# Kernel tuning notes

Hardware: AMD Instinct MI355X
Metric: run time of the kernel (lower is better)

Reference implementation:

```python
import jax, jax.numpy as jnp
import numpy as np

DIM = 512
N = 131072


def _linear_params(key, dim):
    # torch nn.Linear default init: U(-1/sqrt(in), 1/sqrt(in)) for W and b
    kw, kb = jax.random.split(key)
    bound = 1.0 / np.sqrt(dim)
    W = jax.random.uniform(kw, (dim, dim), jnp.float32, -bound, bound)
    b = jax.random.uniform(kb, (dim,), jnp.float32, -bound, bound)
    return W, b


def setup_inputs() -> dict:
    key = jax.random.key(0)
    ks = jax.random.split(key, 8)
    x = jax.random.normal(ks[0], (N, DIM), jnp.float32)
    h = jax.random.normal(ks[1], (N, DIM), jnp.float32)
    W_rx, b_rx = _linear_params(ks[2], DIM)
    W_rh, b_rh = _linear_params(ks[3], DIM)
    W_zx, b_zx = _linear_params(ks[4], DIM)
    W_zh, b_zh = _linear_params(ks[5], DIM)
    W_nx, b_nx = _linear_params(ks[6], DIM)
    W_nh, b_nh = _linear_params(ks[7], DIM)
    return {
        "x": x, "h": h,
        "W_rx": W_rx, "b_rx": b_rx, "W_rh": W_rh, "b_rh": b_rh,
        "W_zx": W_zx, "b_zx": b_zx, "W_zh": W_zh, "b_zh": b_zh,
        "W_nx": W_nx, "b_nx": b_nx, "W_nh": W_nh, "b_nh": b_nh,
    }


def reference(x, h, W_rx, b_rx, W_rh, b_rh, W_zx, b_zx, W_zh, b_zh,
              W_nx, b_nx, W_nh, b_nh):
    # torch Linear: y = x @ W.T + b  (W stored [out, in])
    r = jax.nn.sigmoid(x @ W_rx.T + b_rx + h @ W_rh.T + b_rh)
    z = jax.nn.sigmoid(x @ W_zx.T + b_zx + h @ W_zh.T + b_zh)
    n = jnp.tanh(x @ W_nx.T + b_nx + (r * h) @ W_nh.T + b_nh)
    return (1.0 - z) * n + z * h
```

## Files before the change

### kernel.cpp

```cpp
#include <hip/hip_runtime.h>

#define DIM 512
#define NROWS 131072

typedef __attribute__((ext_vector_type(8))) __bf16 bf16x8;
typedef __attribute__((ext_vector_type(4))) float f32x4;

__device__ __forceinline__ unsigned short f2bf(float f) {
  unsigned u = __builtin_bit_cast(unsigned, f);
  return (unsigned short)((u + 0x7FFFu + ((u >> 16) & 1u)) >> 16);
}
__device__ __forceinline__ float bf2f(unsigned short u) {
  return __builtin_bit_cast(float, (unsigned)u << 16);
}

__device__ __forceinline__ f32x4 mfma16(bf16x8 a, bf16x8 b, f32x4 c) {
  return __builtin_amdgcn_mfma_f32_16x16x32_bf16(a, b, c, 0, 0, 0);
}

__device__ __forceinline__ float sigmoid_fast(float v) {
  return 1.0f / (1.0f + __expf(-v));
}
__device__ __forceinline__ float tanh_fast(float v) {
  float e = __expf(2.0f * v);
  return 1.0f - 2.0f / (e + 1.0f);
}

__device__ __forceinline__ void gl2lds(const unsigned char* g, unsigned char* l) {
  __builtin_amdgcn_global_load_lds(
      (const __attribute__((address_space(1))) unsigned int*)g,
      (__attribute__((address_space(3))) unsigned int*)l, 16, 0, 0);
}

__global__ void prepack_weights(const float* __restrict__ W0, const float* __restrict__ W1,
                                const float* __restrict__ W2, const float* __restrict__ W3,
                                const float* __restrict__ W4, const float* __restrict__ W5,
                                unsigned short* __restrict__ out) {
  int idx = blockIdx.x * 256 + threadIdx.x;
  int e = idx & 7;
  int l = (idx >> 3) & 63;
  int c = (idx >> 9) & 31;
  int f = (idx >> 14) & 15;
  int g = idx >> 18;
  const float* W = (g == 0) ? W0 : (g == 1) ? W1 : (g == 2) ? W2
                 : (g == 3) ? W3 : (g == 4) ? W4 : W5;
  int row = c * 16 + (l & 15);
  int kk  = f * 32 + ((l >> 4) << 3) + e;
  out[idx] = f2bf(W[row * DIM + kk]);
}

#define RH_OFF 65536
#define X_OFF  131072
#define LDS_BYTES 139264

__global__ __launch_bounds__(512, 1)
void gru_fused(const float* __restrict__ x, const float* __restrict__ h,
               const unsigned char* __restrict__ WB,
               const float* __restrict__ b_rx, const float* __restrict__ b_rh,
               const float* __restrict__ b_zx, const float* __restrict__ b_zh,
               const float* __restrict__ b_nx, const float* __restrict__ b_nh,
               float* __restrict__ out) {
  __shared__ __align__(1024) unsigned char lds[LDS_BYTES];

  const int tid  = threadIdx.x;
  const int lane = tid & 63;
  const int w    = tid >> 6;
  const int cfg0 = w * 4;
  const int row0 = blockIdx.x * 64;
  const int lr   = lane & 15;
  const int lk   = lane >> 4;

  auto stageChunk = [&](int g, int f, int dstOff) {
    const unsigned char* src = WB + (size_t)(g * 16 + f) * 32768;
#pragma unroll
    for (int it = 0; it < 4; ++it) {
      int o = (it * 512 + tid) * 16;
      gl2lds(src + o, &lds[dstOff + o]);
    }
  };

  float4 xreg;
  auto loadX = [&](int f) {
    int row = tid >> 3, kq = tid & 7;
    xreg = *(const float4*)(x + (size_t)(row0 + row) * DIM + f * 32 + kq * 4);
  };
  auto writeX = [&](int f) {
    int row = tid >> 3, kq = tid & 7;
    union { unsigned short us[4]; uint2 v; } p;
    p.us[0] = f2bf(xreg.x); p.us[1] = f2bf(xreg.y);
    p.us[2] = f2bf(xreg.z); p.us[3] = f2bf(xreg.w);
    *(uint2*)&lds[X_OFF + (f & 1) * 4096 + (row >> 4) * 1024
                  + ((kq >> 1) * 16 + (row & 15)) * 16 + (kq & 1) * 8] = p.v;
  };

  auto gateStage = [&](int abase, int bbase, f32x4 (&A)[4][4]) {
    bf16x8 af[4], bfr[4];
#pragma unroll
    for (int rf = 0; rf < 4; ++rf)
      af[rf] = *(const bf16x8*)&lds[abase + rf * 1024 + lane * 16];
#pragma unroll
    for (int cf = 0; cf < 4; ++cf)
      bfr[cf] = *(const bf16x8*)&lds[bbase + (cfg0 + cf) * 1024 + lane * 16];
#pragma unroll
    for (int rf = 0; rf < 4; ++rf)
#pragma unroll
      for (int cf = 0; cf < 4; ++cf)
        A[rf][cf] = mfma16(af[rf], bfr[cf], A[rf][cf]);
  };

  f32x4 accR[4][4] = {}, accZ[4][4] = {};

#pragma unroll
  for (int it = 0; it < 16; ++it) {
    int i = tid + it * 512;
    int row = i >> 7, kf4 = i & 127;
    int k = kf4 * 4;
    float4 hv4 = *(const float4*)(h + (size_t)(row0 + row) * DIM + k);
    union { unsigned short us[4]; uint2 v; } p;
    p.us[0] = f2bf(hv4.x); p.us[1] = f2bf(hv4.y);
    p.us[2] = f2bf(hv4.z); p.us[3] = f2bf(hv4.w);
    *(uint2*)&lds[(k >> 5) * 4096 + (row >> 4) * 1024
                  + (((k >> 3) & 3) * 16 + (row & 15)) * 16 + (k & 4) * 2] = p.v;
  }
  loadX(0); writeX(0);
  stageChunk(0, 0, RH_OFF);
  __syncthreads();

#pragma unroll 1
  for (int f = 0; f < 16; ++f) {
    const int xoff = X_OFF + (f & 1) * 4096;
    const int hoff = f * 4096;
    stageChunk(1, f, RH_OFF + 32768);
    if (f < 15) loadX(f + 1);
    gateStage(xoff, RH_OFF, accR);
    __syncthreads();
    stageChunk(2, f, RH_OFF);
    gateStage(xoff, RH_OFF + 32768, accZ);
    __syncthreads();
    stageChunk(3, f, RH_OFF + 32768);
    if (f < 15) writeX(f + 1);
    gateStage(hoff, RH_OFF, accR);
    __syncthreads();
    if (f < 15) stageChunk(0, f + 1, RH_OFF);
    gateStage(hoff, RH_OFF + 32768, accZ);
    __syncthreads();
  }

#pragma unroll
  for (int cf = 0; cf < 4; ++cf) {
    const int col  = (cfg0 + cf) * 16 + lr;
    const float bs = b_rx[col] + b_rh[col];
    const int fcol  = col >> 5;
    const int l2b   = ((col >> 3) & 3) * 16;
    const int ebyte = (col & 7) * 2;
#pragma unroll
    for (int rf = 0; rf < 4; ++rf) {
#pragma unroll
      for (int j = 0; j < 4; ++j) {
        const int rsub = lk * 4 + j;
        unsigned short hu = *(const unsigned short*)
            &lds[fcol * 4096 + rf * 1024 + (l2b + rsub) * 16 + ebyte];
        float rv = sigmoid_fast(accR[rf][cf][j] + bs);
        *(unsigned short*)
            &lds[RH_OFF + fcol * 4096 + rf * 1024 + (l2b + rsub) * 16 + ebyte]
            = f2bf(rv * bf2f(hu));
      }
    }
  }
  __syncthreads();

  f32x4 accN[4][4] = {};
  loadX(0); writeX(0);
  stageChunk(4, 0, 0);
  __syncthreads();
#pragma unroll 1
  for (int f = 0; f < 16; ++f) {
    const int xoff = X_OFF + (f & 1) * 4096;
    stageChunk(5, f, 32768);
    if (f < 15) loadX(f + 1);
    gateStage(xoff, 0, accN);
    __syncthreads();
    if (f < 15) { stageChunk(4, f + 1, 0); writeX(f + 1); }
    gateStage(RH_OFF + f * 4096, 32768, accN);
    __syncthreads();
  }

#pragma unroll
  for (int cf = 0; cf < 4; ++cf) {
    const int col  = (cfg0 + cf) * 16 + lr;
    const float bn = b_nx[col] + b_nh[col];
    const float bz = b_zx[col] + b_zh[col];
#pragma unroll
    for (int rf = 0; rf < 4; ++rf) {
#pragma unroll
      for (int j = 0; j < 4; ++j) {
        const int row = rf * 16 + lk * 4 + j;
        const size_t off = (size_t)(row0 + row) * DIM + col;
        float hv = h[off];
        float nv = tanh_fast(accN[rf][cf][j] + bn);
        float zv = sigmoid_fast(accZ[rf][cf][j] + bz);
        out[off] = (1.0f - zv) * nv + zv * hv;
      }
    }
  }
}

extern "C" void kernel_launch(void* const* d_in, const int* in_sizes, int n_in,
                              void* d_out, int out_size, void* d_ws, size_t ws_size,
                              hipStream_t stream) {
  const float* x    = (const float*)d_in[0];
  const float* h    = (const float*)d_in[1];
  const float* W_rx = (const float*)d_in[2];
  const float* b_rx = (const float*)d_in[3];
  const float* W_rh = (const float*)d_in[4];
  const float* b_rh = (const float*)d_in[5];
  const float* W_zx = (const float*)d_in[6];
  const float* b_zx = (const float*)d_in[7];
  const float* W_zh = (const float*)d_in[8];
  const float* b_zh = (const float*)d_in[9];
  const float* W_nx = (const float*)d_in[10];
  const float* b_nx = (const float*)d_in[11];
  const float* W_nh = (const float*)d_in[12];
  const float* b_nh = (const float*)d_in[13];

  unsigned short* wpack = (unsigned short*)d_ws;

  prepack_weights<<<6144, 256, 0, stream>>>(W_rx, W_zx, W_rh, W_zh, W_nx, W_nh, wpack);
  gru_fused<<<NROWS / 64, 512, 0, stream>>>(x, h, (const unsigned char*)wpack,
                                            b_rx, b_rh, b_zx, b_zh, b_nx, b_nh,
                                            (float*)d_out);
}
```

Measured before the change: 766.2 us.

## Split fused GRU kernel into tiled r/z and n GEMM kernels

Replaces the single fused kernel, which runs one 512-thread block per CU over 64 rows and all 512 columns, with two separate GEMM-style kernels. Each uses 128x128 output tiles, double-buffered LDS, and 256 threads, with up to three blocks per CU. The first kernel computes the r and z gates, writing r*h as bf16 to workspace and z into the output buffer. The second computes the n gate and combines it with z and h. The aim is better occupancy and latency hiding, at the cost of extra global traffic for the r*h and z intermediates and for rereading x and h across column tiles.

Measured after the change: 1.221 ms. 59.4% more time.

```diff
diff --git a/kernel.cpp b/kernel.cpp
--- a/kernel.cpp
+++ b/kernel.cpp
@@ -10,14 +10,9 @@
   unsigned u = __builtin_bit_cast(unsigned, f);
   return (unsigned short)((u + 0x7FFFu + ((u >> 16) & 1u)) >> 16);
 }
-__device__ __forceinline__ float bf2f(unsigned short u) {
-  return __builtin_bit_cast(float, (unsigned)u << 16);
-}
-
 __device__ __forceinline__ f32x4 mfma16(bf16x8 a, bf16x8 b, f32x4 c) {
   return __builtin_amdgcn_mfma_f32_16x16x32_bf16(a, b, c, 0, 0, 0);
 }
-
 __device__ __forceinline__ float sigmoid_fast(float v) {
   return 1.0f / (1.0f + __expf(-v));
 }
@@ -25,8 +20,7 @@
   float e = __expf(2.0f * v);
   return 1.0f - 2.0f / (e + 1.0f);
 }
-
-__device__ __forceinline__ void gl2lds(const unsigned char* g, unsigned char* l) {
+__device__ __forceinline__ void gl2lds(const void* g, void* l) {
   __builtin_amdgcn_global_load_lds(
       (const __attribute__((address_space(1))) unsigned int*)g,
       (__attribute__((address_space(3))) unsigned int*)l, 16, 0, 0);
@@ -49,157 +43,204 @@
   out[idx] = f2bf(W[row * DIM + kk]);
 }
 
-#define RH_OFF 65536
-#define X_OFF  131072
-#define LDS_BYTES 139264
-
-__global__ __launch_bounds__(512, 1)
-void gru_fused(const float* __restrict__ x, const float* __restrict__ h,
-               const unsigned char* __restrict__ WB,
-               const float* __restrict__ b_rx, const float* __restrict__ b_rh,
-               const float* __restrict__ b_zx, const float* __restrict__ b_zh,
-               const float* __restrict__ b_nx, const float* __restrict__ b_nh,
-               float* __restrict__ out) {
-  __shared__ __align__(1024) unsigned char lds[LDS_BYTES];
-
-  const int tid  = threadIdx.x;
-  const int lane = tid & 63;
-  const int w    = tid >> 6;
-  const int cfg0 = w * 4;
-  const int row0 = blockIdx.x * 64;
-  const int lr   = lane & 15;
-  const int lk   = lane >> 4;
-
-  auto stageChunk = [&](int g, int f, int dstOff) {
-    const unsigned char* src = WB + (size_t)(g * 16 + f) * 32768;
-#pragma unroll
-    for (int it = 0; it < 4; ++it) {
-      int o = (it * 512 + tid) * 16;
-      gl2lds(src + o, &lds[dstOff + o]);
-    }
-  };
-
-  float4 xreg;
-  auto loadX = [&](int f) {
-    int row = tid >> 3, kq = tid & 7;
-    xreg = *(const float4*)(x + (size_t)(row0 + row) * DIM + f * 32 + kq * 4);
-  };
-  auto writeX = [&](int f) {
-    int row = tid >> 3, kq = tid & 7;
-    union { unsigned short us[4]; uint2 v; } p;
-    p.us[0] = f2bf(xreg.x); p.us[1] = f2bf(xreg.y);
-    p.us[2] = f2bf(xreg.z); p.us[3] = f2bf(xreg.w);
-    *(uint2*)&lds[X_OFF + (f & 1) * 4096 + (row >> 4) * 1024
-                  + ((kq >> 1) * 16 + (row & 15)) * 16 + (kq & 1) * 8] = p.v;
-  };
-
-  auto gateStage = [&](int abase, int bbase, f32x4 (&A)[4][4]) {
+
+__global__ __launch_bounds__(256, 3)
+void gemm_rz(const float* __restrict__ x, const float* __restrict__ h,
+             const unsigned char* __restrict__ WB,
+             const float* __restrict__ b_rx, const float* __restrict__ b_rh,
+             const float* __restrict__ b_zx, const float* __restrict__ b_zh,
+             unsigned short* __restrict__ rhws, float* __restrict__ zout) {
+  __shared__ __align__(1024) unsigned char ldsA[2][8192];
+  __shared__ __align__(1024) unsigned char ldsB[2][8192];
+
+  const int tid = threadIdx.x, lane = tid & 63, w = tid >> 6;
+  const int wr = w & 1, wc = w >> 1, lr = lane & 15, lk = lane >> 4;
+
+  const int bid = blockIdx.x;
+  const int t = (bid & 7) * 1024 + (bid >> 3);
+  const int panel = t >> 3, n = t & 7;
+  const int row0 = panel * 128;
+  const bool isR = (n < 4);
+  const int gx = isR ? 0 : 1, gh = isR ? 2 : 3, c0 = (n & 3) * 8;
+
+  const int srow = tid >> 1, skh = tid & 1;
+
+  float4 ar0, ar1, ar2, ar3;
+  auto issueA = [&](int f) {
+    const float* src = (f < 16) ? x : h;
+    const float* p = src + (size_t)(row0 + srow) * DIM + (f & 15) * 32 + skh * 16;
+    ar0 = ((const float4*)p)[0]; ar1 = ((const float4*)p)[1];
+    ar2 = ((const float4*)p)[2]; ar3 = ((const float4*)p)[3];
+  };
+  auto writeA = [&](int buf) {
+    union { unsigned short us[8]; uint4 v; } p0, p1;
+    p0.us[0]=f2bf(ar0.x); p0.us[1]=f2bf(ar0.y); p0.us[2]=f2bf(ar0.z); p0.us[3]=f2bf(ar0.w);
+    p0.us[4]=f2bf(ar1.x); p0.us[5]=f2bf(ar1.y); p0.us[6]=f2bf(ar1.z); p0.us[7]=f2bf(ar1.w);
+    p1.us[0]=f2bf(ar2.x); p1.us[1]=f2bf(ar2.y); p1.us[2]=f2bf(ar2.z); p1.us[3]=f2bf(ar2.w);
+    p1.us[4]=f2bf(ar3.x); p1.us[5]=f2bf(ar3.y); p1.us[6]=f2bf(ar3.z); p1.us[7]=f2bf(ar3.w);
+    const int rf = srow >> 4, r15 = srow & 15;
+    *(uint4*)&ldsA[buf][rf * 1024 + ((skh * 2 + 0) * 16 + r15) * 16] = p0.v;
+    *(uint4*)&ldsA[buf][rf * 1024 + ((skh * 2 + 1) * 16 + r15) * 16] = p1.v;
+  };
+  auto stageB = [&](int g, int fk, int buf) {
+    const unsigned char* s = WB + ((size_t)((g * 16 + fk) * 32 + c0) << 10);
+    gl2lds(s + tid * 16, &ldsB[buf][tid * 16]);
+    gl2lds(s + 4096 + tid * 16, &ldsB[buf][4096 + tid * 16]);
+  };
+
+  f32x4 acc[4][4] = {};
+  auto compute = [&](int buf) {
     bf16x8 af[4], bfr[4];
 #pragma unroll
     for (int rf = 0; rf < 4; ++rf)
-      af[rf] = *(const bf16x8*)&lds[abase + rf * 1024 + lane * 16];
+      af[rf] = *(const bf16x8*)&ldsA[buf][(wr * 4 + rf) * 1024 + lane * 16];
 #pragma unroll
     for (int cf = 0; cf < 4; ++cf)
-      bfr[cf] = *(const bf16x8*)&lds[bbase + (cfg0 + cf) * 1024 + lane * 16];
+      bfr[cf] = *(const bf16x8*)&ldsB[buf][(wc * 4 + cf) * 1024 + lane * 16];
+    __builtin_amdgcn_s_setprio(1);
 #pragma unroll
     for (int rf = 0; rf < 4; ++rf)
 #pragma unroll
       for (int cf = 0; cf < 4; ++cf)
-        A[rf][cf] = mfma16(af[rf], bfr[cf], A[rf][cf]);
-  };
-
-  f32x4 accR[4][4] = {}, accZ[4][4] = {};
-
-#pragma unroll
-  for (int it = 0; it < 16; ++it) {
-    int i = tid + it * 512;
-    int row = i >> 7, kf4 = i & 127;
-    int k = kf4 * 4;
-    float4 hv4 = *(const float4*)(h + (size_t)(row0 + row) * DIM + k);
-    union { unsigned short us[4]; uint2 v; } p;
-    p.us[0] = f2bf(hv4.x); p.us[1] = f2bf(hv4.y);
-    p.us[2] = f2bf(hv4.z); p.us[3] = f2bf(hv4.w);
-    *(uint2*)&lds[(k >> 5) * 4096 + (row >> 4) * 1024
-                  + (((k >> 3) & 3) * 16 + (row & 15)) * 16 + (k & 4) * 2] = p.v;
-  }
-  loadX(0); writeX(0);
-  stageChunk(0, 0, RH_OFF);
-  __syncthreads();
-
-#pragma unroll 1
-  for (int f = 0; f < 16; ++f) {
-    const int xoff = X_OFF + (f & 1) * 4096;
-    const int hoff = f * 4096;
-    stageChunk(1, f, RH_OFF + 32768);
-    if (f < 15) loadX(f + 1);
-    gateStage(xoff, RH_OFF, accR);
-    __syncthreads();
-    stageChunk(2, f, RH_OFF);
-    gateStage(xoff, RH_OFF + 32768, accZ);
-    __syncthreads();
-    stageChunk(3, f, RH_OFF + 32768);
-    if (f < 15) writeX(f + 1);
-    gateStage(hoff, RH_OFF, accR);
-    __syncthreads();
-    if (f < 15) stageChunk(0, f + 1, RH_OFF);
-    gateStage(hoff, RH_OFF + 32768, accZ);
-    __syncthreads();
-  }
-
-#pragma unroll
-  for (int cf = 0; cf < 4; ++cf) {
-    const int col  = (cfg0 + cf) * 16 + lr;
-    const float bs = b_rx[col] + b_rh[col];
-    const int fcol  = col >> 5;
-    const int l2b   = ((col >> 3) & 3) * 16;
-    const int ebyte = (col & 7) * 2;
-#pragma unroll
-    for (int rf = 0; rf < 4; ++rf) {
-#pragma unroll
-      for (int j = 0; j < 4; ++j) {
-        const int rsub = lk * 4 + j;
-        unsigned short hu = *(const unsigned short*)
-            &lds[fcol * 4096 + rf * 1024 + (l2b + rsub) * 16 + ebyte];
-        float rv = sigmoid_fast(accR[rf][cf][j] + bs);
-        *(unsigned short*)
-            &lds[RH_OFF + fcol * 4096 + rf * 1024 + (l2b + rsub) * 16 + ebyte]
-            = f2bf(rv * bf2f(hu));
-      }
-    }
-  }
-  __syncthreads();
-
-  f32x4 accN[4][4] = {};
-  loadX(0); writeX(0);
-  stageChunk(4, 0, 0);
+        acc[rf][cf] = mfma16(af[rf], bfr[cf], acc[rf][cf]);
+    __builtin_amdgcn_s_setprio(0);
+  };
+
+  issueA(0); stageB(gx, 0, 0); writeA(0);
   __syncthreads();
 #pragma unroll 1
-  for (int f = 0; f < 16; ++f) {
-    const int xoff = X_OFF + (f & 1) * 4096;
-    stageChunk(5, f, 32768);
-    if (f < 15) loadX(f + 1);
-    gateStage(xoff, 0, accN);
+  for (int f = 0; f < 32; ++f) {
+    const int buf = f & 1;
+    if (f < 31) {
+      const int fn = f + 1;
+      issueA(fn);
+      stageB((fn < 16) ? gx : gh, fn & 15, buf ^ 1);
+    }
+    compute(buf);
+    if (f < 31) writeA(buf ^ 1);
     __syncthreads();
-    if (f < 15) { stageChunk(4, f + 1, 0); writeX(f + 1); }
-    gateStage(RH_OFF + f * 4096, 32768, accN);
+  }
+
+  const float* bx = isR ? b_rx : b_zx;
+  const float* bh = isR ? b_rh : b_zh;
+#pragma unroll
+  for (int cf = 0; cf < 4; ++cf) {
+    const int col = ((n & 3) * 8 + wc * 4 + cf) * 16 + lr;
+    const float bsum = bx[col] + bh[col];
+#pragma unroll
+    for (int rf = 0; rf < 4; ++rf) {
+#pragma unroll
+      for (int j = 0; j < 4; ++j) {
+        const int row = row0 + wr * 64 + rf * 16 + lk * 4 + j;
+        const size_t off = (size_t)row * DIM + col;
+        const float v = acc[rf][cf][j] + bsum;
+        if (isR) rhws[off] = f2bf(sigmoid_fast(v) * h[off]);
+        else     zout[off] = sigmoid_fast(v);
+      }
+    }
+  }
+}
+
+__global__ __launch_bounds__(256, 3)
+void gemm_n(const float* __restrict__ x, const float* __restrict__ h,
+            const unsigned char* __restrict__ WB,
+            const unsigned short* __restrict__ rhws,
+            const float* __restrict__ b_nx, const float* __restrict__ b_nh,
+            float* __restrict__ out) {
+  __shared__ __align__(1024) unsigned char ldsA[2][8192];
+  __shared__ __align__(1024) unsigned char ldsB[2][8192];
+
+  const int tid = threadIdx.x, lane = tid & 63, w = tid >> 6;
+  const int wr = w & 1, wc = w >> 1, lr = lane & 15, lk = lane >> 4;
+
+  const int bid = blockIdx.x;
+  const int t = (bid & 7) * 512 + (bid >> 3);
+  const int panel = t >> 2, n = t & 3;
+  const int row0 = panel * 128;
+  const int c0 = n * 8;
+
+  const int srow = tid >> 1, skh = tid & 1;
+
+  float4 ar0, ar1, ar2, ar3;
+  auto issueA = [&](int fk) {
+    const float* p = x + (size_t)(row0 + srow) * DIM + fk * 32 + skh * 16;
+    ar0 = ((const float4*)p)[0]; ar1 = ((const float4*)p)[1];
+    ar2 = ((const float4*)p)[2]; ar3 = ((const float4*)p)[3];
+  };
+  auto writeA = [&](int buf) {
+    union { unsigned short us[8]; uint4 v; } p0, p1;
+    p0.us[0]=f2bf(ar0.x); p0.us[1]=f2bf(ar0.y); p0.us[2]=f2bf(ar0.z); p0.us[3]=f2bf(ar0.w);
+    p0.us[4]=f2bf(ar1.x); p0.us[5]=f2bf(ar1.y); p0.us[6]=f2bf(ar1.z); p0.us[7]=f2bf(ar1.w);
+    p1.us[0]=f2bf(ar2.x); p1.us[1]=f2bf(ar2.y); p1.us[2]=f2bf(ar2.z); p1.us[3]=f2bf(ar2.w);
+    p1.us[4]=f2bf(ar3.x); p1.us[5]=f2bf(ar3.y); p1.us[6]=f2bf(ar3.z); p1.us[7]=f2bf(ar3.w);
+    const int rf = srow >> 4, r15 = srow & 15;
+    *(uint4*)&ldsA[buf][rf * 1024 + ((skh * 2 + 0) * 16 + r15) * 16] = p0.v;
+    *(uint4*)&ldsA[buf][rf * 1024 + ((skh * 2 + 1) * 16 + r15) * 16] = p1.v;
+  };
+  auto stageRH = [&](int fk, int buf) {
+#pragma unroll
+    for (int it = 0; it < 2; ++it) {
+      const int cell = it * 256 + tid;
+      const int rf = cell >> 6, l = cell & 63;
+      const int row = rf * 16 + (l & 15);
+      const unsigned short* s = rhws + (size_t)(row0 + row) * DIM
+                                + fk * 32 + ((l >> 4) & 3) * 8;
+      gl2lds(s, &ldsA[buf][cell * 16]);
+    }
+  };
+  auto stageB = [&](int g, int fk, int buf) {
+    const unsigned char* s = WB + ((size_t)((g * 16 + fk) * 32 + c0) << 10);
+    gl2lds(s + tid * 16, &ldsB[buf][tid * 16]);
+    gl2lds(s + 4096 + tid * 16, &ldsB[buf][4096 + tid * 16]);
+  };
+
+  f32x4 acc[4][4] = {};
+  auto compute = [&](int buf) {
+    bf16x8 af[4], bfr[4];
+#pragma unroll
+    for (int rf = 0; rf < 4; ++rf)
+      af[rf] = *(const bf16x8*)&ldsA[buf][(wr * 4 + rf) * 1024 + lane * 16];
+#pragma unroll
+    for (int cf = 0; cf < 4; ++cf)
+      bfr[cf] = *(const bf16x8*)&ldsB[buf][(wc * 4 + cf) * 1024 + lane * 16];
+    __builtin_amdgcn_s_setprio(1);
+#pragma unroll
+    for (int rf = 0; rf < 4; ++rf)
+#pragma unroll
+      for (int cf = 0; cf < 4; ++cf)
+        acc[rf][cf] = mfma16(af[rf], bfr[cf], acc[rf][cf]);
+    __builtin_amdgcn_s_setprio(0);
+  };
+
+  issueA(0); stageB(4, 0, 0); writeA(0);
+  __syncthreads();
+#pragma unroll 1
+  for (int f = 0; f < 32; ++f) {
+    const int buf = f & 1;
+    const int fn = f + 1;
+    if (f < 31) {
+      if (fn < 16) issueA(fn);
+      stageB((fn < 16) ? 4 : 5, fn & 15, buf ^ 1);
+      if (fn >= 16) stageRH(fn & 15, buf ^ 1);
+    }
+    compute(buf);
+    if (f < 31 && fn < 16) writeA(buf ^ 1);
     __syncthreads();
   }
 
 #pragma unroll
   for (int cf = 0; cf < 4; ++cf) {
-    const int col  = (cfg0 + cf) * 16 + lr;
+    const int col = (n * 8 + wc * 4 + cf) * 16 + lr;
     const float bn = b_nx[col] + b_nh[col];
-    const float bz = b_zx[col] + b_zh[col];
 #pragma unroll
     for (int rf = 0; rf < 4; ++rf) {
 #pragma unroll
       for (int j = 0; j < 4; ++j) {
-        const int row = rf * 16 + lk * 4 + j;
-        const size_t off = (size_t)(row0 + row) * DIM + col;
-        float hv = h[off];
-        float nv = tanh_fast(accN[rf][cf][j] + bn);
-        float zv = sigmoid_fast(accZ[rf][cf][j] + bz);
-        out[off] = (1.0f - zv) * nv + zv * hv;
+        const int row = row0 + wr * 64 + rf * 16 + lk * 4 + j;
+        const size_t off = (size_t)row * DIM + col;
+        const float nv = tanh_fast(acc[rf][cf][j] + bn);
+        const float zv = out[off];
+        out[off] = (1.0f - zv) * nv + zv * h[off];
       }
     }
   }
@@ -223,10 +264,13 @@
   const float* W_nh = (const float*)d_in[12];
   const float* b_nh = (const float*)d_in[13];
 
-  unsigned short* wpack = (unsigned short*)d_ws;
+  unsigned char* ws = (unsigned char*)d_ws;
+  unsigned short* wpack = (unsigned short*)ws;
+  unsigned short* rhws  = (unsigned short*)(ws + (4ull << 20));
 
   prepack_weights<<<6144, 256, 0, stream>>>(W_rx, W_zx, W_rh, W_zh, W_nx, W_nh, wpack);
-  gru_fused<<<NROWS / 64, 512, 0, stream>>>(x, h, (const unsigned char*)wpack,
-                                            b_rx, b_rh, b_zx, b_zh, b_nx, b_nh,
-                                            (float*)d_out);
-}
+  gemm_rz<<<8192, 256, 0, stream>>>(x, h, (const unsigned char*)wpack,
+                                    b_rx, b_rh, b_zx, b_zh, rhws, (float*)d_out);
+  gemm_n<<<4096, 256, 0, stream>>>(x, h, (const unsigned char*)wpack,
+                                   rhws, b_nx, b_nh, (float*)d_out);
+}
```
